# Kernel optimization log

Hardware: AMD Instinct MI355X
Metric: run time of the kernel (lower is better)

## Reference

```python
import jax, jax.numpy as jnp
import numpy as np
from jax import lax

B, T = 512, 64
IN, H, V1, P = 256, 512, 101, 8  # input_size, rnn_size, vocab_size+1, max_param
CLS, REG = 512, 512


def setup_inputs() -> dict:
    key = jax.random.key(0)
    ks = jax.random.split(key, 20)
    u = lambda k, s: jax.random.uniform(k, s, jnp.float32, -0.1, 0.1)
    sh = 1.0 / np.sqrt(H)
    ul = lambda k, s: jax.random.uniform(k, s, jnp.float32, -sh, sh)
    return {
        "x": jax.random.normal(ks[0], (B, IN), jnp.float32),
        "y": jax.random.randint(ks[1], (B, T), 0, V1),
        "embed": u(ks[2], (V1, IN)),
        "w_ih0": ul(ks[3], (4 * H, IN)),
        "w_hh0": ul(ks[4], (4 * H, H)),
        "w_ih1": ul(ks[5], (4 * H, H)),
        "w_hh1": ul(ks[6], (4 * H, H)),
        "l1w": u(ks[7], (CLS, H)), "l1b": jnp.zeros((CLS,), jnp.float32),
        "l2w": u(ks[8], (V1, CLS)), "l2b": jnp.zeros((V1,), jnp.float32),
        "r1w": u(ks[9], (REG, H)), "r1b": jnp.zeros((REG,), jnp.float32),
        "r2w": u(ks[10], (V1 * P, V1 + REG)), "r2b": jnp.zeros((V1 * P,), jnp.float32),
    }


def _cell(xi, h, c, wih, whh):
    g = xi @ wih.T + h @ whh.T          # [B, 4H], gate order i,f,g,o (no bias)
    i, f, gg, o = jnp.split(g, 4, axis=-1)
    c = jax.nn.sigmoid(f) * c + jax.nn.sigmoid(i) * jnp.tanh(gg)
    h = jax.nn.sigmoid(o) * jnp.tanh(c)
    return h, c


def reference(x, y, embed, w_ih0, w_hh0, w_ih1, w_hh1,
              l1w, l1b, l2w, l2b, r1w, r1b, r2w, r2b):
    # teacher forcing (sample_prob=0): step-0 input is x, step-i input is embed(y[:, i-1])
    emb = embed[y[:, :-1]]                                  # [B, T-1, IN]
    xt = jnp.concatenate([x[None], jnp.transpose(emb, (1, 0, 2))], axis=0)  # [T, B, IN]

    z = jnp.zeros((x.shape[0], H), x.dtype)

    def step(carry, xi):
        h0, c0, h1, c1 = carry
        h0, c0 = _cell(xi, h0, c0, w_ih0, w_hh0)
        h1, c1 = _cell(h0, h1, c1, w_ih1, w_hh1)
        return (h0, c0, h1, c1), h1

    _, outs = lax.scan(step, (z, z, z, z), xt)              # [T, B, H]

    feat2 = jax.nn.relu(outs @ l1w.T + l1b) @ l2w.T + l2b   # [T, B, V1]
    pgm_score = jax.nn.log_softmax(feat2, axis=-1)
    trans_prob = lax.stop_gradient(jax.nn.softmax(feat2, axis=-1))
    pf1 = jax.nn.relu(outs @ r1w.T + r1b)                   # [T, B, REG]
    ps = (jnp.concatenate([trans_prob, pf1], axis=-1) @ r2w.T + r2b)
    ps = ps.reshape(T, -1, V1, P)                           # [T, B, V1, P]
    idx = y.T                                               # [T, B]
    param = ps[jnp.arange(T)[:, None], jnp.arange(x.shape[0])[None, :], idx]  # [T, B, P]
    return (jnp.transpose(pgm_score, (1, 0, 2)),            # [B, T, V1]
            jnp.transpose(param, (1, 0, 2)))                # [B, T, P]
```

## Files before the change

kernel.cpp:

```cpp
#include <hip/hip_runtime.h>
#include <stdint.h>

typedef unsigned short u16;
typedef short bf16x8 __attribute__((ext_vector_type(8)));
typedef float f32x4 __attribute__((ext_vector_type(4)));
typedef int i32x4 __attribute__((ext_vector_type(4)));

#define DEV static __device__ __forceinline__

constexpr int B_ = 512, T_ = 64, IN_ = 256, H_ = 512, V1_ = 101, P_ = 8, G4_ = 2048;
constexpr int EXR = 613;
constexpr int M_  = T_ * B_;
constexpr int NBLK = 256;

DEV float b2f(u16 u) { union { uint32_t i; float f; } v; v.i = ((uint32_t)u) << 16; return v.f; }
DEV u16 f2b(float f) {
  union { float f; uint32_t i; } v; v.f = f;
  uint32_t i = v.i;
  return (u16)((i + 0x7fffu + ((i >> 16) & 1u)) >> 16);
}
DEV float sigf(float x) { return 1.f / (1.f + __expf(-x)); }
DEV float tanh_(float x) {
  float c = fminf(fmaxf(x, -15.f), 15.f);
  float e = __expf(2.f * c);
  return (e - 1.f) / (e + 1.f);
}
DEV bf16x8 ld8(const u16* p) { return *reinterpret_cast<const bf16x8*>(p); }
DEV f32x4 mfma16(bf16x8 a, bf16x8 b, f32x4 c) {
  return __builtin_amdgcn_mfma_f32_16x16x32_bf16(a, b, c, 0, 0, 0);
}

struct CvtArgs {
  const float* src[9];
  u16* dst[9];
  int pre[10];
};

__global__ __launch_bounds__(256) void k_cvtall(CvtArgs a) {
  int gid = blockIdx.x * 256 + threadIdx.x;
  if (gid >= a.pre[9]) return;
  int s = 0;
#pragma unroll
  for (int i = 1; i < 9; ++i) s += (gid >= a.pre[i]);
  const int local = gid - a.pre[s];
  const float4 v = reinterpret_cast<const float4*>(a.src[s])[local];
  ushort4 o;
  o.x = f2b(v.x); o.y = f2b(v.y); o.z = f2b(v.z); o.w = f2b(v.w);
  reinterpret_cast<ushort4*>(a.dst[s])[local] = o;
}

__global__ __launch_bounds__(256) void k_precomp(const u16* __restrict__ ex_src,
                                                 const u16* __restrict__ wih0b,
                                                 float* __restrict__ EX0) {
  const int lane = threadIdx.x & 63;
  const int wv = threadIdx.x >> 6;
  const int m0 = blockIdx.x * 64 + wv * 16;
  const int n0 = blockIdx.y * 64;
  const int lr = lane & 15;
  const int lk = (lane >> 4) * 8;

  const int arow = m0 + lr;
  const bool valid = arow < EXR;

  f32x4 acc[4] = {};
  for (int k0 = 0; k0 < IN_; k0 += 32) {
    bf16x8 a = {};
    if (valid) a = ld8(ex_src + (size_t)arow * IN_ + k0 + lk);
#pragma unroll
    for (int c = 0; c < 4; ++c) {
      bf16x8 b = ld8(wih0b + (size_t)(n0 + c * 16 + lr) * IN_ + k0 + lk);
      acc[c] = mfma16(a, b, acc[c]);
    }
  }
  const int rb = (lane >> 4) * 4;
#pragma unroll
  for (int c = 0; c < 4; ++c)
#pragma unroll
    for (int r = 0; r < 4; ++r) {
      int row = m0 + rb + r;
      int col = n0 + c * 16 + (lane & 15);
      if (row < EXR) EX0[(size_t)row * G4_ + col] = acc[c][r];
    }
}

DEV int lds_off(int row, int kcol ) {
  return row * 1024 + ((kcol * 2) ^ ((row & 7) << 4));
}

__global__ __launch_bounds__(512, 1) void k_scan(
    const u16* __restrict__ whh0, const u16* __restrict__ wih1, const u16* __restrict__ whh1,
    const float* __restrict__ EX0, const int* __restrict__ y,
    u16* h0buf, u16* h1buf, unsigned* flags ) {
  __shared__ u16 h0s[16 * 512];
  __shared__ u16 h1s[16 * 512];
  __shared__ u16 stage0[16][64];
  __shared__ u16 stage1[16][64];
  const size_t BH = (size_t)B_ * H_;
  const int tid = threadIdx.x;
  const int lane = tid & 63;
  const int wv = tid >> 6;
  const int q = wv & 3;
  const bool isL1 = wv >= 4;
  const int bm = blockIdx.x >> 3;
  const int bj = blockIdx.x & 7;
  const int lr = lane & 15;
  const int lk = (lane >> 4) * 8;
  const int col = bj * 64 + q * 16 + lr;
  const int rb = (lane >> 4) * 4;
  const int lcol = q * 16 + lr;

  const u16* wp[8];
#pragma unroll
  for (int g = 0; g < 4; ++g) {
    if (!isL1) {
      wp[g] = whh0 + (size_t)(g * H_ + col) * H_ + lk;
      wp[4 + g] = whh0 + (size_t)(g * H_ + col) * H_ + lk;
    } else {
      wp[g] = wih1 + (size_t)(g * H_ + col) * H_ + lk;
      wp[4 + g] = whh1 + (size_t)(g * H_ + col) * H_ + lk;
    }
  }
  f32x4 cst = {};
  unsigned* gflags = flags + bm * 8;

  for (int k = 0; k <= T_; ++k) {
    {
      const u16* h0g = h0buf + (size_t)k * BH + (size_t)(bm * 16) * H_;
#pragma unroll
      for (int rr = 0; rr < 2; ++rr) {
        const int idx = rr * 512 + tid;
        const int row = idx >> 6, cc = idx & 63;
        i32x4 d = *(const i32x4*)(h0g + (size_t)row * H_ + cc * 8);
        *(i32x4*)((char*)h0s + row * 1024 + ((cc * 16) ^ ((row & 7) << 4))) = d;
      }
      if (k >= 1) {
        const u16* h1g = h1buf + (size_t)(k - 1) * BH + (size_t)(bm * 16) * H_;
#pragma unroll
        for (int rr = 0; rr < 2; ++rr) {
          const int idx = rr * 512 + tid;
          const int row = idx >> 6, cc = idx & 63;
          i32x4 d = *(const i32x4*)(h1g + (size_t)row * H_ + cc * 8);
          *(i32x4*)((char*)h1s + row * 1024 + ((cc * 16) ^ ((row & 7) << 4))) = d;
        }
      }
    }
    __syncthreads();

    if (!isL1) {
      if (k < T_) {
        f32x4 acc[4] = {};
#pragma unroll
        for (int i = 0; i < 16; ++i) {
          bf16x8 a0 = *(const bf16x8*)((const char*)h0s + lds_off(lr, i * 32 + lk));
#pragma unroll
          for (int g = 0; g < 4; ++g) acc[g] = mfma16(a0, ld8(wp[g] + i * 32), acc[g]);
        }
#pragma unroll
        for (int r = 0; r < 4; ++r) {
          const int row = bm * 16 + rb + r;
          const int srow = (k == 0) ? (V1_ + row) : y[row * T_ + k - 1];
          const float* bp = EX0 + (size_t)srow * G4_ + col;
          float iv = acc[0][r] + bp[0], fv = acc[1][r] + bp[H_];
          float gv = acc[2][r] + bp[2 * H_], ov = acc[3][r] + bp[3 * H_];
          float cn = sigf(fv) * cst[r] + sigf(iv) * tanh_(gv);
          cst[r] = cn;
          stage0[rb + r][lcol] = f2b(sigf(ov) * tanh_(cn));
        }
      }
    } else {
      if (k >= 1) {
        f32x4 acc[4] = {};
#pragma unroll
        for (int i = 0; i < 16; ++i) {
          bf16x8 a0 = *(const bf16x8*)((const char*)h0s + lds_off(lr, i * 32 + lk));
          bf16x8 a1 = *(const bf16x8*)((const char*)h1s + lds_off(lr, i * 32 + lk));
#pragma unroll
          for (int g = 0; g < 4; ++g) {
            acc[g] = mfma16(a0, ld8(wp[g] + i * 32), acc[g]);
            acc[g] = mfma16(a1, ld8(wp[4 + g] + i * 32), acc[g]);
          }
        }
#pragma unroll
        for (int r = 0; r < 4; ++r) {
          float cn = sigf(acc[1][r]) * cst[r] + sigf(acc[0][r]) * tanh_(acc[2][r]);
          cst[r] = cn;
          stage1[rb + r][lcol] = f2b(sigf(acc[3][r]) * tanh_(cn));
        }
      }
    }
    __syncthreads();

    if (tid < 256) {
      if (tid < 128) {
        if (k < T_) {
          const int lrow = tid >> 3, c8 = (tid & 7) * 8;
          i32x4 d = *(const i32x4*)&stage0[lrow][c8];
          u16* gp = h0buf + (size_t)(k + 1) * BH + (size_t)(bm * 16 + lrow) * H_ + bj * 64 + c8;
          asm volatile("global_store_dwordx4 %0, %1, off sc0 sc1" :: "v"(gp), "v"(d) : "memory");
        }
      } else {
        if (k >= 1) {
          const int t2 = tid - 128;
          const int lrow = t2 >> 3, c8 = (t2 & 7) * 8;
          i32x4 d = *(const i32x4*)&stage1[lrow][c8];
          u16* gp = h1buf + (size_t)k * BH + (size_t)(bm * 16 + lrow) * H_ + bj * 64 + c8;
          asm volatile("global_store_dwordx4 %0, %1, off sc0 sc1" :: "v"(gp), "v"(d) : "memory");
        }
      }
    }
    asm volatile("s_waitcnt vmcnt(0)" ::: "memory");
    __syncthreads();
    if (wv == 0) {
      const unsigned tgt = (unsigned)(k + 1);
      if (lane == 0)
        __hip_atomic_store(&gflags[bj], tgt, __ATOMIC_RELAXED, __HIP_MEMORY_SCOPE_AGENT);
      for (;;) {
        unsigned v = __hip_atomic_load(&gflags[lane & 7], __ATOMIC_RELAXED, __HIP_MEMORY_SCOPE_AGENT);
        if (__all(v >= tgt)) break;
        __builtin_amdgcn_s_sleep(1);
      }
    }
    __syncthreads();
    asm volatile("" ::: "memory");
  }
}

__global__ __launch_bounds__(256) void k_fused1(const u16* __restrict__ outs,
                                                const u16* __restrict__ l1w, const float* __restrict__ l1b,
                                                const u16* __restrict__ r1w, const float* __restrict__ r1b,
                                                u16* __restrict__ feat1, u16* __restrict__ pf1) {
  const int lane = threadIdx.x & 63;
  const int wv = threadIdx.x >> 6;
  const int lr = lane & 15;
  const int lk = (lane >> 4) * 8;
  const int ar = blockIdx.x * 64 + wv * 16 + lr;
  const int rb = (lane >> 4) * 4;
  const int row0 = blockIdx.x * 64 + wv * 16 + rb;

  bf16x8 a[16];
  {
    const u16* ap = outs + (size_t)ar * H_ + lk;
#pragma unroll
    for (int i = 0; i < 16; ++i) a[i] = ld8(ap + i * 32);
  }
  for (int w = 0; w < 2; ++w) {
    const u16* W = w ? r1w : l1w;
    const float* bias = w ? r1b : l1b;
    u16* dst = w ? pf1 : feat1;
    for (int nc = 0; nc < 4; ++nc) {
      f32x4 acc[8] = {};
#pragma unroll
      for (int i = 0; i < 16; ++i)
#pragma unroll
        for (int n = 0; n < 8; ++n)
          acc[n] = mfma16(a[i], ld8(W + (size_t)(nc * 128 + n * 16 + lr) * H_ + i * 32 + lk), acc[n]);
#pragma unroll
      for (int n = 0; n < 8; ++n) {
        const int colc = nc * 128 + n * 16 + lr;
        const float bv = bias[colc];
#pragma unroll
        for (int r = 0; r < 4; ++r)
          dst[(size_t)(row0 + r) * H_ + colc] = f2b(fmaxf(acc[n][r] + bv, 0.f));
      }
    }
  }
}

__global__ __launch_bounds__(256) void k_fused2(const u16* __restrict__ feat1,
                                                const u16* __restrict__ l2w, const float* __restrict__ l2b,
                                                const u16* __restrict__ pf1,
                                                const float* __restrict__ r2w, const float* __restrict__ r2b,
                                                const int* __restrict__ y,
                                                float* __restrict__ pgm, float* __restrict__ par) {
  __shared__ float trans[64][104];
  const int lane = threadIdx.x & 63;
  const int wv = threadIdx.x >> 6;
  const int lr = lane & 15;
  const int lk = (lane >> 4) * 8;
  const int ar = blockIdx.x * 64 + wv * 16 + lr;
  const int rb = (lane >> 4) * 4;

  f32x4 acc[7] = {};
  {
    const u16* ap = feat1 + (size_t)ar * H_ + lk;
#pragma unroll
    for (int i = 0; i < 16; ++i) {
      bf16x8 av = ld8(ap + i * 32);
#pragma unroll
      for (int c = 0; c < 7; ++c) {
        const int n = c * 16 + lr;
        bf16x8 b = {};
        if (n < V1_) b = ld8(l2w + (size_t)n * H_ + i * 32 + lk);
        acc[c] = mfma16(av, b, acc[c]);
      }
    }
  }
#pragma unroll
  for (int r = 0; r < 4; ++r) {
    float v[7];
    float mx = -1e30f;
#pragma unroll
    for (int c = 0; c < 7; ++c) {
      const int colc = c * 16 + lr;
      v[c] = (colc < V1_) ? acc[c][r] + l2b[colc] : -1e30f;
      mx = fmaxf(mx, v[c]);
    }
#pragma unroll
    for (int o = 1; o < 16; o <<= 1) mx = fmaxf(mx, __shfl_xor(mx, o, 64));
    float e[7], s = 0.f;
#pragma unroll
    for (int c = 0; c < 7; ++c) { e[c] = (c * 16 + lr < V1_) ? __expf(v[c] - mx) : 0.f; s += e[c]; }
#pragma unroll
    for (int o = 1; o < 16; o <<= 1) s += __shfl_xor(s, o, 64);
    const float lz = __logf(s), inv = 1.f / s;
    const int m = blockIdx.x * 64 + wv * 16 + rb + r;
    const int t = m >> 9, bb = m & 511;
    float* po = pgm + ((size_t)bb * T_ + t) * V1_;
#pragma unroll
    for (int c = 0; c < 7; ++c) {
      const int colc = c * 16 + lr;
      if (colc < V1_) { po[colc] = v[c] - mx - lz; trans[wv * 16 + rb + r][colc] = e[c] * inv; }
    }
  }
  __syncthreads();
  for (int rr = 0; rr < 16; ++rr) {
    const int m = blockIdx.x * 64 + wv * 16 + rr;
    const int t = m >> 9, bb = m & 511;
    const int idx = y[bb * T_ + t];
    const float* wb = r2w + (size_t)idx * P_ * 613;
    float a8[P_] = {};
    for (int kk = lane; kk < 613; kk += 64) {
      float xv = (kk < V1_) ? trans[wv * 16 + rr][kk] : b2f(pf1[(size_t)m * H_ + kk - V1_]);
#pragma unroll
      for (int p = 0; p < P_; ++p) a8[p] += xv * wb[(size_t)p * 613 + kk];
    }
#pragma unroll
    for (int p = 0; p < P_; ++p)
#pragma unroll
      for (int o = 1; o < 64; o <<= 1) a8[p] += __shfl_xor(a8[p], o, 64);
    if (lane < P_) par[((size_t)bb * T_ + t) * P_ + lane] = a8[lane] + r2b[idx * P_ + lane];
  }
}

extern "C" void kernel_launch(void* const* d_in, const int* in_sizes, int n_in,
                              void* d_out, int out_size, void* d_ws, size_t ws_size,
                              hipStream_t stream) {
  (void)in_sizes; (void)n_in; (void)out_size; (void)ws_size;
  const float* x     = (const float*)d_in[0];
  const int*   y     = (const int*)d_in[1];
  const float* embed = (const float*)d_in[2];
  const float* wih0  = (const float*)d_in[3];
  const float* whh0  = (const float*)d_in[4];
  const float* wih1  = (const float*)d_in[5];
  const float* whh1  = (const float*)d_in[6];
  const float* l1w   = (const float*)d_in[7];
  const float* l1b   = (const float*)d_in[8];
  const float* l2w   = (const float*)d_in[9];
  const float* l2b   = (const float*)d_in[10];
  const float* r1w   = (const float*)d_in[11];
  const float* r1b   = (const float*)d_in[12];
  const float* r2w   = (const float*)d_in[13];
  const float* r2b   = (const float*)d_in[14];

  float* out_pgm = (float*)d_out;
  float* out_par = out_pgm + (size_t)B_ * T_ * V1_;

  char* ws = (char*)d_ws;
  size_t off = 0;
  auto alloc = [&](size_t bytes) { void* p = ws + off; off += (bytes + 255) & ~(size_t)255; return p; };

  const size_t BH2 = (size_t)B_ * H_ * 2;

  unsigned* flags = (unsigned*)alloc(NBLK * 4);
  u16* h0buf  = (u16*)alloc((size_t)(T_ + 1) * BH2);
  u16* h1buf  = (u16*)alloc((size_t)(T_ + 1) * BH2);

  float* EX0   = (float*)alloc((size_t)EXR * G4_ * 4);
  u16* ex_src  = (u16*)alloc((size_t)EXR * IN_ * 2);
  u16* wih0b   = (u16*)alloc((size_t)4 * H_ * IN_ * 2);
  u16* whh0b   = (u16*)alloc((size_t)4 * H_ * H_ * 2);
  u16* wih1b   = (u16*)alloc((size_t)4 * H_ * H_ * 2);
  u16* whh1b   = (u16*)alloc((size_t)4 * H_ * H_ * 2);
  u16* l1wb    = (u16*)alloc((size_t)H_ * H_ * 2);
  u16* r1wb    = (u16*)alloc((size_t)H_ * H_ * 2);
  u16* l2wb    = (u16*)alloc((size_t)V1_ * H_ * 2);
  u16* feat1   = (u16*)alloc((size_t)M_ * H_ * 2);
  u16* pf1     = (u16*)alloc((size_t)M_ * H_ * 2);

  (void)hipMemsetAsync(flags, 0, NBLK * 4 + BH2, stream);
  (void)hipMemsetAsync(h1buf, 0, BH2, stream);

  CvtArgs ca;
  const float* srcs[9] = {embed, x, wih0, whh0, wih1, whh1, l1w, r1w, l2w};
  u16* dsts[9] = {ex_src, ex_src + (size_t)V1_ * IN_, wih0b, whh0b, wih1b, whh1b, l1wb, r1wb, l2wb};
  int ns[9] = {V1_ * IN_, B_ * IN_, 4 * H_ * IN_, 4 * H_ * H_, 4 * H_ * H_, 4 * H_ * H_,
               H_ * H_, H_ * H_, V1_ * H_};
  int acc4 = 0;
  for (int i = 0; i < 9; ++i) {
    ca.src[i] = srcs[i]; ca.dst[i] = dsts[i]; ca.pre[i] = acc4; acc4 += ns[i] / 4;
  }
  ca.pre[9] = acc4;
  k_cvtall<<<(acc4 + 255) / 256, 256, 0, stream>>>(ca);

  k_precomp<<<dim3(10, 32), 256, 0, stream>>>(ex_src, wih0b, EX0);

  k_scan<<<NBLK, 512, 0, stream>>>(whh0b, wih1b, whh1b, EX0, y, h0buf, h1buf, flags);

  u16* outs = h1buf + (size_t)B_ * H_;
  k_fused1<<<512, 256, 0, stream>>>(outs, l1wb, l1b, r1wb, r1b, feat1, pf1);
  k_fused2<<<512, 256, 0, stream>>>(feat1, l2wb, l2b, pf1, r2w, r2b, y, out_pgm, out_par);
}
```

Measured before the change: 2.053 ms.

## Split LSTM layers into separate blocks with producer-consumer flag sync

The persistent scan kernel used to put both LSTM layers in one 512-thread block and run a full barrier across the 8 column blocks after every step. Now 512 blocks of 256 threads each own a single layer, and each step waits only on the specific flags it depends on: layer 0 waits for its own row group's previous h0, layer 1 waits for the current h0 and its previous h1. This is meant to let layer 0 run ahead of layer 1 and to drop the global wait at the end of each step. It needs all 512 blocks to be co-resident at once, or the spin-waits will deadlock.

```diff
diff --git a/kernel.cpp b/kernel.cpp
--- a/kernel.cpp
+++ b/kernel.cpp
@@ -11,7 +11,6 @@
 constexpr int B_ = 512, T_ = 64, IN_ = 256, H_ = 512, V1_ = 101, P_ = 8, G4_ = 2048;
 constexpr int EXR = 613;
 constexpr int M_  = T_ * B_;
-constexpr int NBLK = 256;
 
 DEV float b2f(u16 u) { union { uint32_t i; float f; } v; v.i = ((uint32_t)u) << 16; return v.f; }
 DEV u16 f2b(float f) {
@@ -83,61 +82,64 @@
     }
 }
 
-DEV int lds_off(int row, int kcol ) {
-  return row * 1024 + ((kcol * 2) ^ ((row & 7) << 4));
-}
-
-__global__ __launch_bounds__(512, 1) void k_scan(
+__global__ __launch_bounds__(256, 1) void k_scan(
     const u16* __restrict__ whh0, const u16* __restrict__ wih1, const u16* __restrict__ whh1,
     const float* __restrict__ EX0, const int* __restrict__ y,
     u16* h0buf, u16* h1buf, unsigned* flags ) {
   __shared__ u16 h0s[16 * 512];
   __shared__ u16 h1s[16 * 512];
-  __shared__ u16 stage0[16][64];
-  __shared__ u16 stage1[16][64];
+  __shared__ u16 stg[16][64];
   const size_t BH = (size_t)B_ * H_;
   const int tid = threadIdx.x;
   const int lane = tid & 63;
   const int wv = tid >> 6;
-  const int q = wv & 3;
-  const bool isL1 = wv >= 4;
-  const int bm = blockIdx.x >> 3;
+  const int isL1 = blockIdx.x >> 8;
+  const int bm = (blockIdx.x >> 3) & 31;
   const int bj = blockIdx.x & 7;
   const int lr = lane & 15;
   const int lk = (lane >> 4) * 8;
-  const int col = bj * 64 + q * 16 + lr;
+  const int col = bj * 64 + wv * 16 + lr;
   const int rb = (lane >> 4) * 4;
-  const int lcol = q * 16 + lr;
-
-  const u16* wp[8];
+  const int lcol = wv * 16 + lr;
+
+  const u16* wpa[4]; const u16* wpb[4];
 #pragma unroll
   for (int g = 0; g < 4; ++g) {
-    if (!isL1) {
-      wp[g] = whh0 + (size_t)(g * H_ + col) * H_ + lk;
-      wp[4 + g] = whh0 + (size_t)(g * H_ + col) * H_ + lk;
-    } else {
-      wp[g] = wih1 + (size_t)(g * H_ + col) * H_ + lk;
-      wp[4 + g] = whh1 + (size_t)(g * H_ + col) * H_ + lk;
-    }
+    wpa[g] = (isL1 ? wih1 : whh0) + (size_t)(g * H_ + col) * H_ + lk;
+    wpb[g] = (isL1 ? whh1 : whh0) + (size_t)(g * H_ + col) * H_ + lk;
   }
   f32x4 cst = {};
-  unsigned* gflags = flags + bm * 8;
-
-  for (int k = 0; k <= T_; ++k) {
+  unsigned* gf = flags + bm * 16;
+  const int npoll = isL1 ? 16 : 8;
+
+  for (int k = 0; k < T_; ++k) {
+    if (wv == 0 && (k > 0 || isL1)) {
+      const unsigned thr = (lane < 8) ? (unsigned)(isL1 ? k + 1 : k)
+                                      : ((lane < 16 && isL1) ? (unsigned)k : 0u);
+      for (;;) {
+        unsigned v = 0xffffffffu;
+        if (lane < npoll)
+          v = __hip_atomic_load(&gf[lane], __ATOMIC_RELAXED, __HIP_MEMORY_SCOPE_AGENT);
+        if (__all(v >= thr)) break;
+        __builtin_amdgcn_s_sleep(1);
+      }
+    }
+    __syncthreads();
+
     {
-      const u16* h0g = h0buf + (size_t)k * BH + (size_t)(bm * 16) * H_;
-#pragma unroll
-      for (int rr = 0; rr < 2; ++rr) {
-        const int idx = rr * 512 + tid;
+      const u16* h0g = h0buf + (size_t)(k + isL1) * BH + (size_t)(bm * 16) * H_;
+#pragma unroll
+      for (int rr = 0; rr < 4; ++rr) {
+        const int idx = rr * 256 + tid;
         const int row = idx >> 6, cc = idx & 63;
         i32x4 d = *(const i32x4*)(h0g + (size_t)row * H_ + cc * 8);
         *(i32x4*)((char*)h0s + row * 1024 + ((cc * 16) ^ ((row & 7) << 4))) = d;
       }
-      if (k >= 1) {
-        const u16* h1g = h1buf + (size_t)(k - 1) * BH + (size_t)(bm * 16) * H_;
-#pragma unroll
-        for (int rr = 0; rr < 2; ++rr) {
-          const int idx = rr * 512 + tid;
+      if (isL1) {
+        const u16* h1g = h1buf + (size_t)k * BH + (size_t)(bm * 16) * H_;
+#pragma unroll
+        for (int rr = 0; rr < 4; ++rr) {
+          const int idx = rr * 256 + tid;
           const int row = idx >> 6, cc = idx & 63;
           i32x4 d = *(const i32x4*)(h1g + (size_t)row * H_ + cc * 8);
           *(i32x4*)((char*)h1s + row * 1024 + ((cc * 16) ^ ((row & 7) << 4))) = d;
@@ -147,81 +149,58 @@
     __syncthreads();
 
     if (!isL1) {
-      if (k < T_) {
-        f32x4 acc[4] = {};
-#pragma unroll
-        for (int i = 0; i < 16; ++i) {
-          bf16x8 a0 = *(const bf16x8*)((const char*)h0s + lds_off(lr, i * 32 + lk));
-#pragma unroll
-          for (int g = 0; g < 4; ++g) acc[g] = mfma16(a0, ld8(wp[g] + i * 32), acc[g]);
+      f32x4 acc[4] = {};
+#pragma unroll
+      for (int i = 0; i < 16; ++i) {
+        bf16x8 a0 = *(const bf16x8*)((const char*)h0s + lr * 1024 + (((i * 32 + lk) * 2) ^ ((lr & 7) << 4)));
+#pragma unroll
+        for (int g = 0; g < 4; ++g) acc[g] = mfma16(a0, ld8(wpa[g] + i * 32), acc[g]);
+      }
+#pragma unroll
+      for (int r = 0; r < 4; ++r) {
+        const int row = bm * 16 + rb + r;
+        const int srow = (k == 0) ? (V1_ + row) : y[row * T_ + k - 1];
+        const float* bp = EX0 + (size_t)srow * G4_ + col;
+        float iv = acc[0][r] + bp[0], fv = acc[1][r] + bp[H_];
+        float gv = acc[2][r] + bp[2 * H_], ov = acc[3][r] + bp[3 * H_];
+        float cn = sigf(fv) * cst[r] + sigf(iv) * tanh_(gv);
+        cst[r] = cn;
+        stg[rb + r][lcol] = f2b(sigf(ov) * tanh_(cn));
+      }
+    } else {
+      f32x4 acc[4] = {};
+#pragma unroll
+      for (int i = 0; i < 16; ++i) {
+        const int so = ((i * 32 + lk) * 2) ^ ((lr & 7) << 4);
+        bf16x8 a0 = *(const bf16x8*)((const char*)h0s + lr * 1024 + so);
+        bf16x8 a1 = *(const bf16x8*)((const char*)h1s + lr * 1024 + so);
+#pragma unroll
+        for (int g = 0; g < 4; ++g) {
+          acc[g] = mfma16(a0, ld8(wpa[g] + i * 32), acc[g]);
+          acc[g] = mfma16(a1, ld8(wpb[g] + i * 32), acc[g]);
         }
-#pragma unroll
-        for (int r = 0; r < 4; ++r) {
-          const int row = bm * 16 + rb + r;
-          const int srow = (k == 0) ? (V1_ + row) : y[row * T_ + k - 1];
-          const float* bp = EX0 + (size_t)srow * G4_ + col;
-          float iv = acc[0][r] + bp[0], fv = acc[1][r] + bp[H_];
-          float gv = acc[2][r] + bp[2 * H_], ov = acc[3][r] + bp[3 * H_];
-          float cn = sigf(fv) * cst[r] + sigf(iv) * tanh_(gv);
-          cst[r] = cn;
-          stage0[rb + r][lcol] = f2b(sigf(ov) * tanh_(cn));
-        }
-      }
-    } else {
-      if (k >= 1) {
-        f32x4 acc[4] = {};
-#pragma unroll
-        for (int i = 0; i < 16; ++i) {
-          bf16x8 a0 = *(const bf16x8*)((const char*)h0s + lds_off(lr, i * 32 + lk));
-          bf16x8 a1 = *(const bf16x8*)((const char*)h1s + lds_off(lr, i * 32 + lk));
-#pragma unroll
-          for (int g = 0; g < 4; ++g) {
-            acc[g] = mfma16(a0, ld8(wp[g] + i * 32), acc[g]);
-            acc[g] = mfma16(a1, ld8(wp[4 + g] + i * 32), acc[g]);
-          }
-        }
-#pragma unroll
-        for (int r = 0; r < 4; ++r) {
-          float cn = sigf(acc[1][r]) * cst[r] + sigf(acc[0][r]) * tanh_(acc[2][r]);
-          cst[r] = cn;
-          stage1[rb + r][lcol] = f2b(sigf(acc[3][r]) * tanh_(cn));
-        }
+      }
+#pragma unroll
+      for (int r = 0; r < 4; ++r) {
+        float cn = sigf(acc[1][r]) * cst[r] + sigf(acc[0][r]) * tanh_(acc[2][r]);
+        cst[r] = cn;
+        stg[rb + r][lcol] = f2b(sigf(acc[3][r]) * tanh_(cn));
       }
     }
     __syncthreads();
 
-    if (tid < 256) {
-      if (tid < 128) {
-        if (k < T_) {
-          const int lrow = tid >> 3, c8 = (tid & 7) * 8;
-          i32x4 d = *(const i32x4*)&stage0[lrow][c8];
-          u16* gp = h0buf + (size_t)(k + 1) * BH + (size_t)(bm * 16 + lrow) * H_ + bj * 64 + c8;
-          asm volatile("global_store_dwordx4 %0, %1, off sc0 sc1" :: "v"(gp), "v"(d) : "memory");
-        }
-      } else {
-        if (k >= 1) {
-          const int t2 = tid - 128;
-          const int lrow = t2 >> 3, c8 = (t2 & 7) * 8;
-          i32x4 d = *(const i32x4*)&stage1[lrow][c8];
-          u16* gp = h1buf + (size_t)k * BH + (size_t)(bm * 16 + lrow) * H_ + bj * 64 + c8;
-          asm volatile("global_store_dwordx4 %0, %1, off sc0 sc1" :: "v"(gp), "v"(d) : "memory");
-        }
-      }
+    if (tid < 128) {
+      const int lrow = tid >> 3, c8 = (tid & 7) * 8;
+      i32x4 d = *(const i32x4*)&stg[lrow][c8];
+      u16* base = isL1 ? h1buf : h0buf;
+      u16* gp = base + (size_t)(k + 1) * BH + (size_t)(bm * 16 + lrow) * H_ + bj * 64 + c8;
+      asm volatile("global_store_dwordx4 %0, %1, off sc0 sc1" :: "v"(gp), "v"(d) : "memory");
     }
     asm volatile("s_waitcnt vmcnt(0)" ::: "memory");
     __syncthreads();
-    if (wv == 0) {
-      const unsigned tgt = (unsigned)(k + 1);
-      if (lane == 0)
-        __hip_atomic_store(&gflags[bj], tgt, __ATOMIC_RELAXED, __HIP_MEMORY_SCOPE_AGENT);
-      for (;;) {
-        unsigned v = __hip_atomic_load(&gflags[lane & 7], __ATOMIC_RELAXED, __HIP_MEMORY_SCOPE_AGENT);
-        if (__all(v >= tgt)) break;
-        __builtin_amdgcn_s_sleep(1);
-      }
-    }
-    __syncthreads();
-    asm volatile("" ::: "memory");
+    if (tid == 0)
+      __hip_atomic_store(&gf[isL1 * 8 + bj], (unsigned)(k + 1),
+                         __ATOMIC_RELAXED, __HIP_MEMORY_SCOPE_AGENT);
   }
 }
 
@@ -371,7 +350,7 @@
 
   const size_t BH2 = (size_t)B_ * H_ * 2;
 
-  unsigned* flags = (unsigned*)alloc(NBLK * 4);
+  unsigned* flags = (unsigned*)alloc(32 * 16 * 4);
   u16* h0buf  = (u16*)alloc((size_t)(T_ + 1) * BH2);
   u16* h1buf  = (u16*)alloc((size_t)(T_ + 1) * BH2);
 
@@ -387,7 +366,7 @@
   u16* feat1   = (u16*)alloc((size_t)M_ * H_ * 2);
   u16* pf1     = (u16*)alloc((size_t)M_ * H_ * 2);
 
-  (void)hipMemsetAsync(flags, 0, NBLK * 4 + BH2, stream);
+  (void)hipMemsetAsync(flags, 0, 32 * 16 * 4 + BH2, stream);
   (void)hipMemsetAsync(h1buf, 0, BH2, stream);
 
   CvtArgs ca;
@@ -404,7 +383,7 @@
 
   k_precomp<<<dim3(10, 32), 256, 0, stream>>>(ex_src, wih0b, EX0);
 
-  k_scan<<<NBLK, 512, 0, stream>>>(whh0b, wih1b, whh1b, EX0, y, h0buf, h1buf, flags);
+  k_scan<<<512, 256, 0, stream>>>(whh0b, wih1b, whh1b, EX0, y, h0buf, h1buf, flags);
 
   u16* outs = h1buf + (size_t)B_ * H_;
   k_fused1<<<512, 256, 0, stream>>>(outs, l1wb, l1b, r1wb, r1b, feat1, pf1);
```

After: 2.089 ms. Within noise of the previous version (+1.8%).
